# Kernel optimization log

Hardware: AMD Instinct MI355X
Metric: run time of the kernel (lower is better)

Reference implementation:

```python
import jax, jax.numpy as jnp
import numpy as np

QK_I2_S = 128  # weights per block; 32 packed bytes per block
RMS_EPS = 1e-6  # RMSNorm default eps (BitNetMLP builds RMSNorm without eps arg)


def unpack_simd(packed, K):
    """Unpack SIMD block-interleaved 2-bit weights to float {-1,0,1,2}-1 values.

    packed: [M, K//4] uint8. Within each 128-weight block (32 bytes):
      byte[j] bits 6:7 -> w[j+0], 4:5 -> w[j+32], 2:3 -> w[j+64], 0:1 -> w[j+96].
    """
    M = packed.shape[0]
    nb = K // QK_I2_S
    b = packed.astype(jnp.int32).reshape(M, nb, 32)
    # stack shift groups so flattened order is [j+0..31, j+32.., j+64.., j+96..]
    w = jnp.stack([(b >> 6) & 3, (b >> 4) & 3, (b >> 2) & 3, b & 3], axis=2)  # [M,nb,4,32]
    return w.reshape(M, K).astype(jnp.float32) - 1.0


def setup_inputs() -> dict:
    key = jax.random.key(0)
    ks = jax.random.split(key, 8)
    H, I = 2560, 6912
    B, S = 4, 2048
    x = jax.random.normal(ks[0], (B, S, H), dtype=jnp.float32)
    gate_packed = jax.random.randint(ks[1], (I, H // 4), 0, 256, dtype=jnp.int32).astype(jnp.uint8)
    up_packed = jax.random.randint(ks[2], (I, H // 4), 0, 256, dtype=jnp.int32).astype(jnp.uint8)
    down_packed = jax.random.randint(ks[3], (H, I // 4), 0, 256, dtype=jnp.int32).astype(jnp.uint8)
    gate_scale = jax.random.uniform(ks[4], (1,), minval=0.01, maxval=0.1, dtype=jnp.float32)
    up_scale = jax.random.uniform(ks[5], (1,), minval=0.01, maxval=0.1, dtype=jnp.float32)
    down_scale = jax.random.uniform(ks[6], (1,), minval=0.01, maxval=0.1, dtype=jnp.float32)
    norm_w = jnp.ones((I,), dtype=jnp.float32) + 0.05 * jax.random.normal(ks[7], (I,), dtype=jnp.float32)
    return {"x": x, "gate_packed": gate_packed, "gate_scale": gate_scale,
            "up_packed": up_packed, "up_scale": up_scale,
            "down_packed": down_packed, "down_scale": down_scale,
            "norm_w": norm_w}


def reference(x, gate_packed, gate_scale, up_packed, up_scale, down_packed, down_scale, norm_w):
    H = x.shape[-1]
    I = norm_w.shape[0]
    # BitLinear (fallback path math): unpack ternary weights, apply scalar weight scale
    Wg = unpack_simd(gate_packed, H) * gate_scale[0]   # [I, H]
    Wu = unpack_simd(up_packed, H) * up_scale[0]       # [I, H]
    Wd = unpack_simd(down_packed, I) * down_scale[0]   # [H, I]
    gate = jnp.einsum('bsh,ih->bsi', x, Wg)
    up = jnp.einsum('bsh,ih->bsi', x, Wu)
    hidden = jnp.square(jax.nn.relu(gate)) * up        # ReLU^2 gating
    # RMSNorm over intermediate dim
    var = jnp.mean(jnp.square(hidden), axis=-1, keepdims=True)
    hidden = norm_w * (hidden * jax.lax.rsqrt(var + RMS_EPS))
    return jnp.einsum('bsi,hi->bsh', hidden, Wd)
```

## Files before the change

### kernel.cpp

```cpp
#include <hip/hip_runtime.h>
#include <cstdint>
#include <cstddef>

#define H_DIM 2560
#define I_DIM 6912
#define NTOK  8192

typedef __attribute__((ext_vector_type(8))) __bf16 bf16x8;
typedef __attribute__((ext_vector_type(4))) float  f32x4;

__device__ inline void gld16(void* lds, const void* g) {
    __builtin_amdgcn_global_load_lds(
        (__attribute__((address_space(1))) void*)(void*)g,
        (__attribute__((address_space(3))) void*)lds, 16, 0, 0);
}

__global__ __launch_bounds__(256) void cvt_x_kernel(const float* __restrict__ x,
                                                    __bf16* __restrict__ xb, int n8) {
    int gid = blockIdx.x * 256 + threadIdx.x;
    if (gid >= n8) return;
    const float4* p = (const float4*)(x + (size_t)gid * 8);
    float4 v0 = p[0], v1 = p[1];
    bf16x8 o;
    o[0] = (__bf16)v0.x; o[1] = (__bf16)v0.y; o[2] = (__bf16)v0.z; o[3] = (__bf16)v0.w;
    o[4] = (__bf16)v1.x; o[5] = (__bf16)v1.y; o[6] = (__bf16)v1.z; o[7] = (__bf16)v1.w;
    *(bf16x8*)(xb + (size_t)gid * 8) = o;
}

__global__ __launch_bounds__(256) void unpack_w_kernel(const int* __restrict__ packed,
                                                       __bf16* __restrict__ out,
                                                       int M, int K,
                                                       const float* __restrict__ norm,
                                                       int mode) {
    int gid = blockIdx.x * 256 + threadIdx.x;
    int per_row = K >> 3;
    if (gid >= M * per_row) return;
    int i  = gid / per_row;
    int k0 = (gid % per_row) * 8;
    int blk = k0 >> 7;
    int grp = (k0 >> 5) & 3;
    int j0  = k0 & 31;
    int shift = 6 - 2 * grp;
    const int* p = packed + (size_t)i * (K >> 2) + blk * 32 + j0;
    int4 v0 = *(const int4*)p;
    int4 v1 = *(const int4*)(p + 4);
    int vals[8] = {v0.x, v0.y, v0.z, v0.w, v1.x, v1.y, v1.z, v1.w};
    bf16x8 o;
#pragma unroll
    for (int b = 0; b < 8; ++b) {
        float f = (float)(((vals[b] >> shift) & 3) - 1);
        if (norm) f *= norm[k0 + b];
        o[b] = (__bf16)f;
    }
    int dst = (mode == 0) ? i : ((i >> 4) * 32 + (i & 15) + ((mode == 2) ? 16 : 0));
    *(bf16x8*)(out + (size_t)dst * K + k0) = o;
}

__global__ __launch_bounds__(256) void rms_rs_kernel(const __bf16* __restrict__ hidden,
                                                     float* __restrict__ rs) {
    const int tk = blockIdx.x;
    const __bf16* row = hidden + (size_t)tk * I_DIM;
    float s = 0.f;
    for (int idx = threadIdx.x; idx < I_DIM / 8; idx += 256) {
        bf16x8 v = *(const bf16x8*)&row[idx * 8];
#pragma unroll
        for (int j = 0; j < 8; ++j) { float f = (float)v[j]; s += f * f; }
    }
#pragma unroll
    for (int off = 32; off; off >>= 1) s += __shfl_down(s, off, 64);
    __shared__ float wsum[4];
    if ((threadIdx.x & 63) == 0) wsum[threadIdx.x >> 6] = s;
    __syncthreads();
    if (threadIdx.x == 0) {
        float tot = wsum[0] + wsum[1] + wsum[2] + wsum[3];
        rs[tk] = rsqrtf(tot / (float)I_DIM + 1e-6f);
    }
}

template<int KDIM>
__global__ __launch_bounds__(512, 2) void gemm_gu8(
    const __bf16* __restrict__ A,
    const __bf16* __restrict__ B,
    const float* __restrict__ gs_p,
    const float* __restrict__ us_p,
    __bf16* __restrict__ hidden,
    int nby)
{
    constexpr int KB = KDIM * 2;
    constexpr int NT = KDIM / 64;
    __shared__ __align__(16) char smem[131072];

    const int nwg = (int)gridDim.x;
    const int q = nwg >> 3;
    const int id = (int)blockIdx.x;
    const int wg = (id & 7) * q + (id >> 3);
    const int bx = wg / nby, by = wg % nby;
    const int m0 = bx * 256, n0 = by * 256;

    const int t = (int)threadIdx.x;
    const int lane = t & 63;
    const int wid = t >> 6;
    const int wm = wid >> 2, wn = wid & 3;
    const int l15 = lane & 15, s8 = lane >> 4;

    const int qa  = (t & 7) ^ ((t >> 3) & 7);
    const int rA2 = ((t >> 3) << 1) + (qa >> 2);
    const char* gA0 = (const char*)A + (size_t)(m0 + rA2) * KB + (qa & 3) * 16;
    const char* gA1 = (const char*)A + (size_t)(m0 + 128 + rA2) * KB + (qa & 3) * 16;
    const int sr0 = t >> 3, sr1 = 64 + (t >> 3);
    const int br0 = ((sr0 >> 5) << 6) + (sr0 & 31);
    const int br1 = ((sr1 >> 5) << 6) + (sr1 & 31);
    const char* gB0 = (const char*)B + (size_t)(n0 + br0) * KB + qa * 16;
    const char* gB1 = (const char*)B + (size_t)(n0 + br1) * KB + qa * 16;
    char* ldst = smem + t * 16;

    const int aoff = (wm * 64 + (l15 >> 1)) * 128 +
                     (((((l15 & 1) << 2) | s8) ^ ((l15 >> 1) & 7)) << 4);
    const int boff = (wn * 32 + l15) * 128;
    const int bco0 = ((s8) ^ (l15 & 7)) << 4;
    const int bco1 = ((4 | s8) ^ (l15 & 7)) << 4;

    f32x4 acc[8][4];
#pragma unroll
    for (int f = 0; f < 8; ++f)
#pragma unroll
        for (int n = 0; n < 4; ++n) acc[f][n] = (f32x4){0, 0, 0, 0};

#define STG_A(d, kt, kk) do {                                              \
        size_t _oA = (size_t)(kt) * 128 + (kk) * 64;                       \
        gld16(ldst + (d) * 65536 + (kk) * 16384,        gA0 + _oA);        \
        gld16(ldst + (d) * 65536 + (kk) * 16384 + 8192, gA1 + _oA);        \
    } while (0)
#define STG_B(d, kt, nh) do {                                              \
        size_t _oB = (size_t)(nh) * 32 * KB + (size_t)(kt) * 128;          \
        gld16(ldst + (d) * 65536 + 32768 + (nh) * 16384,        gB0 + _oB);\
        gld16(ldst + (d) * 65536 + 32768 + (nh) * 16384 + 8192, gB1 + _oB);\
    } while (0)
#define LOAD_A(d, kk) do { _Pragma("unroll")                               \
        for (int _f = 0; _f < 8; ++_f)                                     \
            a[_f] = *(const bf16x8*)(smem + (d) * 65536 + (kk) * 16384 +   \
                                     _f * 1024 + aoff); } while (0)
#define LOAD_B(d, nh, bc) do {                                             \
        b0 = *(const bf16x8*)(smem + (d) * 65536 + 32768 + (nh) * 16384 +  \
                              boff + (bc));                                \
        b1 = *(const bf16x8*)(smem + (d) * 65536 + 32768 + (nh) * 16384 +  \
                              boff + (bc) + 2048); } while (0)
#define MFMA16(nh) do { __builtin_amdgcn_s_setprio(1); _Pragma("unroll")   \
        for (int _f = 0; _f < 8; ++_f) {                                   \
            acc[_f][(nh) * 2] = __builtin_amdgcn_mfma_f32_16x16x32_bf16(   \
                a[_f], b0, acc[_f][(nh) * 2], 0, 0, 0);                    \
            acc[_f][(nh) * 2 + 1] = __builtin_amdgcn_mfma_f32_16x16x32_bf16(\
                a[_f], b1, acc[_f][(nh) * 2 + 1], 0, 0, 0); }              \
        __builtin_amdgcn_s_setprio(0); } while (0)
#define BAR() do { asm volatile("" ::: "memory");                          \
        __builtin_amdgcn_s_barrier();                                      \
        asm volatile("" ::: "memory"); } while (0)

    STG_A(0, 0, 0); STG_A(0, 0, 1); STG_B(0, 0, 0); STG_B(0, 0, 1);
    STG_A(1, 1, 0); STG_B(1, 1, 0);
    asm volatile("s_waitcnt vmcnt(4)" ::: "memory");
    BAR();

    bf16x8 a[8], b0, b1;
    for (int kt = 0; kt < NT; ++kt) {
        const int d = kt & 1;
        LOAD_A(d, 0); LOAD_B(d, 0, bco0);
        if (kt + 1 < NT) STG_A(d ^ 1, kt + 1, 1);
        BAR(); MFMA16(0); BAR();
        LOAD_B(d, 1, bco0);
        if (kt + 1 < NT) STG_B(d ^ 1, kt + 1, 1);
        BAR(); MFMA16(1); BAR();
        LOAD_A(d, 1); LOAD_B(d, 0, bco1);
        if (kt + 2 < NT) STG_A(d, kt + 2, 0);
        BAR(); MFMA16(0); BAR();
        LOAD_B(d, 1, bco1);
        if (kt + 2 < NT) {
            STG_B(d, kt + 2, 0);
            asm volatile("s_waitcnt vmcnt(4)" ::: "memory");
        } else {
            asm volatile("s_waitcnt vmcnt(0)" ::: "memory");
        }
        BAR(); MFMA16(1); BAR();
    }

#undef STG_A
#undef STG_B
#undef LOAD_A
#undef LOAD_B
#undef MFMA16
#undef BAR

    const float comb = gs_p[0] * gs_p[0] * us_p[0];
    const int r0 = m0 + wm * 128 + s8 * 4;
#pragma unroll
    for (int f = 0; f < 8; ++f)
#pragma unroll
        for (int p = 0; p < 2; ++p)
#pragma unroll
            for (int j = 0; j < 4; ++j) {
                float g = acc[f][2 * p][j];
                float u = acc[f][2 * p + 1][j];
                float r = fmaxf(g, 0.f);
                hidden[(size_t)(r0 + f * 16 + j) * I_DIM +
                       ((by * 8 + wn * 2 + p) * 16 + l15)] = (__bf16)(comb * r * r * u);
            }
}

template<int KDIM>
__global__ __launch_bounds__(512) void gemm_down_pipe(
    const __bf16* __restrict__ A,
    const __bf16* __restrict__ B,
    const float* __restrict__ ds_p,
    const float* __restrict__ rs,
    float* __restrict__ outf,
    int nby)
{
    constexpr int BM = 256, BN = 128, BK = 64;
    constexpr int NT = KDIM / BK;
    constexpr int SLOTB = (BM + BN) * BK * 2;
    __shared__ __align__(16) char smem[3 * SLOTB];

    const int nwg = (int)gridDim.x;
    const int q = nwg >> 3;
    const int id = (int)blockIdx.x;
    const int wg = (id & 7) * q + (id >> 3);
    const int bx = wg / nby;
    const int by = wg % nby;

    const int m0 = bx * BM;
    const int n0 = by * BN;
    const int t  = (int)threadIdx.x;
    const int lane = t & 63;
    const int wm = (t >> 6) >> 1;
    const int wn = (t >> 6) & 1;

    const int srow = t >> 3;
    const int scol = ((t & 7) * 16) ^ ((srow & 7) << 4);
    const char* gA = (const char*)A + (size_t)(m0 + srow) * (KDIM * 2) + scol;
    const char* gB = (const char*)B + (size_t)(n0 + srow) * (KDIM * 2) + scol;
    char* lbase = smem + t * 16;

    const int l15 = lane & 15;
    const int xv  = (l15 & 7) << 4;
    const int colx[2] = { (((lane >> 4) * 16) ^ xv), ((64 + (lane >> 4) * 16) ^ xv) };

    f32x4 acc[4][4];
#pragma unroll
    for (int a = 0; a < 4; ++a)
#pragma unroll
        for (int b = 0; b < 4; ++b) acc[a][b] = (f32x4){0, 0, 0, 0};

#define STAGE_T(s, kt) do {                                                     \
        char* _ls = lbase + (s) * SLOTB;                                        \
        const char* _ga = gA + (kt) * (BK * 2);                                 \
        _Pragma("unroll")                                                       \
        for (int _i = 0; _i < 4; ++_i)                                          \
            gld16(_ls + _i * 8192, _ga + (size_t)_i * 64 * (KDIM * 2));         \
        const char* _gb = gB + (kt) * (BK * 2);                                 \
        char* _lb = _ls + BM * BK * 2;                                          \
        _Pragma("unroll")                                                       \
        for (int _i = 0; _i < 2; ++_i)                                          \
            gld16(_lb + _i * 8192, _gb + (size_t)_i * 64 * (KDIM * 2));         \
    } while (0)

#define COMPUTE_T(s) do {                                                       \
        const char* _sa = smem + (s) * SLOTB;                                   \
        const char* _sb = _sa + BM * BK * 2;                                    \
        _Pragma("unroll")                                                       \
        for (int _kk = 0; _kk < 2; ++_kk) {                                     \
            bf16x8 _a[4], _b[4];                                                \
            _Pragma("unroll")                                                   \
            for (int _f = 0; _f < 4; ++_f)                                      \
                _a[_f] = *(const bf16x8*)(_sa + (wm * 64 + _f * 16 + l15) * 128 + colx[_kk]); \
            _Pragma("unroll")                                                   \
            for (int _f = 0; _f < 4; ++_f)                                      \
                _b[_f] = *(const bf16x8*)(_sb + (wn * 64 + _f * 16 + l15) * 128 + colx[_kk]); \
            __builtin_amdgcn_s_setprio(1);                                      \
            _Pragma("unroll")                                                   \
            for (int _fm = 0; _fm < 4; ++_fm)                                   \
                _Pragma("unroll")                                               \
                for (int _fn = 0; _fn < 4; ++_fn)                               \
                    acc[_fm][_fn] = __builtin_amdgcn_mfma_f32_16x16x32_bf16(    \
                        _a[_fm], _b[_fn], acc[_fm][_fn], 0, 0, 0);              \
            __builtin_amdgcn_s_setprio(0);                                      \
        }                                                                       \
    } while (0)

    STAGE_T(0, 0);
    STAGE_T(1, 1);
    asm volatile("s_waitcnt vmcnt(6)" ::: "memory");
    __builtin_amdgcn_s_barrier();
    asm volatile("" ::: "memory");

    for (int kt = 0; kt < NT; ++kt) {
        if (kt + 2 < NT) STAGE_T((kt + 2) % 3, kt + 2);
        COMPUTE_T(kt % 3);
        if (kt + 2 < NT) {
            asm volatile("s_waitcnt vmcnt(6)" ::: "memory");
            __builtin_amdgcn_s_barrier();
            asm volatile("" ::: "memory");
        } else if (kt + 2 == NT) {
            asm volatile("s_waitcnt vmcnt(0)" ::: "memory");
            __builtin_amdgcn_s_barrier();
            asm volatile("" ::: "memory");
        }
    }

#undef STAGE_T
#undef COMPUTE_T

    const float ds = ds_p[0];
    const int r0 = m0 + wm * 64 + (lane >> 4) * 4;
#pragma unroll
    for (int fm = 0; fm < 4; ++fm)
#pragma unroll
        for (int j = 0; j < 4; ++j) {
            const int row = r0 + fm * 16 + j;
            const float sc = ds * rs[row];
#pragma unroll
            for (int fn = 0; fn < 4; ++fn)
                outf[(size_t)row * H_DIM + (n0 + wn * 64 + fn * 16 + l15)] =
                    sc * acc[fm][fn][j];
        }
}

extern "C" void kernel_launch(void* const* d_in, const int* in_sizes, int n_in,
                              void* d_out, int out_size, void* d_ws, size_t ws_size,
                              hipStream_t stream) {
    const float* x   = (const float*)d_in[0];
    const int*   gp  = (const int*)d_in[1];
    const float* gs  = (const float*)d_in[2];
    const int*   upk = (const int*)d_in[3];
    const float* us  = (const float*)d_in[4];
    const int*   dp  = (const int*)d_in[5];
    const float* dsc = (const float*)d_in[6];
    const float* nw  = (const float*)d_in[7];
    float* out = (float*)d_out;

    char* ws = (char*)d_ws;
    __bf16* xb     = (__bf16*)ws;  ws += (size_t)NTOK * H_DIM * 2;
    __bf16* bgu    = (__bf16*)ws;  ws += (size_t)2 * I_DIM * H_DIM * 2;
    __bf16* wdb    = (__bf16*)ws;  ws += (size_t)H_DIM * I_DIM * 2;
    __bf16* hidden = (__bf16*)ws;  ws += (size_t)NTOK * I_DIM * 2;
    float*  rsbuf  = (float*)ws;   ws += (size_t)NTOK * 4;

    cvt_x_kernel<<<(NTOK * H_DIM / 8 + 255) / 256, 256, 0, stream>>>(x, xb, NTOK * H_DIM / 8);
    unpack_w_kernel<<<(I_DIM * H_DIM / 8 + 255) / 256, 256, 0, stream>>>(gp, bgu, I_DIM, H_DIM, nullptr, 1);
    unpack_w_kernel<<<(I_DIM * H_DIM / 8 + 255) / 256, 256, 0, stream>>>(upk, bgu, I_DIM, H_DIM, nullptr, 2);
    unpack_w_kernel<<<(H_DIM * I_DIM / 8 + 255) / 256, 256, 0, stream>>>(dp, wdb, H_DIM, I_DIM, nw, 0);

    gemm_gu8<H_DIM><<<dim3((NTOK / 256) * (2 * I_DIM / 256)), 512, 0, stream>>>(
        xb, bgu, gs, us, hidden, 2 * I_DIM / 256);

    rms_rs_kernel<<<NTOK, 256, 0, stream>>>(hidden, rsbuf);

    gemm_down_pipe<I_DIM><<<dim3((NTOK / 256) * (H_DIM / 128)), 512, 0, stream>>>(
        hidden, wdb, dsc, rsbuf, out, H_DIM / 128);
}
```

Before: 855.4 us.

## Switch both GEMMs to 32x32x16 MFMA with matching interleave and LDS layout

Both the gate/up GEMM and the down GEMM now use the 32x32x16 bf16 MFMA instead of 16x16x32. The gate/up weights are interleaved in 32-row groups to match the larger tile. LDS fragment addressing, the staging order and the epilogue row mapping are rewritten for the 32x32 output layout. The larger MFMA does more work per instruction and needs fewer LDS reads per flop. In exchange it changes register pressure and the LDS bank access pattern, and the swizzle must stay correct.

```diff
diff --git a/kernel.cpp b/kernel.cpp
--- a/kernel.cpp
+++ b/kernel.cpp
@@ -8,6 +8,7 @@
 
 typedef __attribute__((ext_vector_type(8))) __bf16 bf16x8;
 typedef __attribute__((ext_vector_type(4))) float  f32x4;
+typedef __attribute__((ext_vector_type(16))) float f32x16;
 
 __device__ inline void gld16(void* lds, const void* g) {
     __builtin_amdgcn_global_load_lds(
@@ -52,7 +53,7 @@
         if (norm) f *= norm[k0 + b];
         o[b] = (__bf16)f;
     }
-    int dst = (mode == 0) ? i : ((i >> 4) * 32 + (i & 15) + ((mode == 2) ? 16 : 0));
+    int dst = (mode == 0) ? i : ((i >> 5) * 64 + (i & 31) + ((mode == 2) ? 32 : 0));
     *(bf16x8*)(out + (size_t)dst * K + k0) = o;
 }
 
@@ -78,7 +79,7 @@
 }
 
 template<int KDIM>
-__global__ __launch_bounds__(512, 2) void gemm_gu8(
+__global__ __launch_bounds__(512, 2) void gemm_gu32(
     const __bf16* __restrict__ A,
     const __bf16* __restrict__ B,
     const float* __restrict__ gs_p,
@@ -101,59 +102,69 @@
     const int lane = t & 63;
     const int wid = t >> 6;
     const int wm = wid >> 2, wn = wid & 3;
-    const int l15 = lane & 15, s8 = lane >> 4;
+    const int l31 = lane & 31, lh = lane >> 5;
 
     const int qa  = (t & 7) ^ ((t >> 3) & 7);
     const int rA2 = ((t >> 3) << 1) + (qa >> 2);
-    const char* gA0 = (const char*)A + (size_t)(m0 + rA2) * KB + (qa & 3) * 16;
-    const char* gA1 = (const char*)A + (size_t)(m0 + 128 + rA2) * KB + (qa & 3) * 16;
-    const int sr0 = t >> 3, sr1 = 64 + (t >> 3);
-    const int br0 = ((sr0 >> 5) << 6) + (sr0 & 31);
-    const int br1 = ((sr1 >> 5) << 6) + (sr1 & 31);
-    const char* gB0 = (const char*)B + (size_t)(n0 + br0) * KB + qa * 16;
-    const char* gB1 = (const char*)B + (size_t)(n0 + br1) * KB + qa * 16;
+    const int cb  = (qa & 3) * 16;
+    const char* gA0 = (const char*)A + (size_t)(m0 + rA2) * KB + cb;
+    const char* gA1 = (const char*)A + (size_t)(m0 + 128 + rA2) * KB + cb;
+    const char* gB0 = (const char*)B + (size_t)(n0 + rA2) * KB + cb;
+    const char* gB1 = (const char*)B + (size_t)(n0 + 128 + rA2) * KB + cb;
     char* ldst = smem + t * 16;
 
-    const int aoff = (wm * 64 + (l15 >> 1)) * 128 +
-                     (((((l15 & 1) << 2) | s8) ^ ((l15 >> 1) & 7)) << 4);
-    const int boff = (wn * 32 + l15) * 128;
-    const int bco0 = ((s8) ^ (l15 & 7)) << 4;
-    const int bco1 = ((4 | s8) ^ (l15 & 7)) << 4;
-
-    f32x4 acc[8][4];
-#pragma unroll
-    for (int f = 0; f < 8; ++f)
-#pragma unroll
-        for (int n = 0; n < 4; ++n) acc[f][n] = (f32x4){0, 0, 0, 0};
-
-#define STG_A(d, kt, kk) do {                                              \
-        size_t _oA = (size_t)(kt) * 128 + (kk) * 64;                       \
-        gld16(ldst + (d) * 65536 + (kk) * 16384,        gA0 + _oA);        \
-        gld16(ldst + (d) * 65536 + (kk) * 16384 + 8192, gA1 + _oA);        \
-    } while (0)
-#define STG_B(d, kt, nh) do {                                              \
-        size_t _oB = (size_t)(nh) * 32 * KB + (size_t)(kt) * 128;          \
-        gld16(ldst + (d) * 65536 + 32768 + (nh) * 16384,        gB0 + _oB);\
-        gld16(ldst + (d) * 65536 + 32768 + (nh) * 16384 + 8192, gB1 + _oB);\
-    } while (0)
-#define LOAD_A(d, kk) do { _Pragma("unroll")                               \
-        for (int _f = 0; _f < 8; ++_f)                                     \
-            a[_f] = *(const bf16x8*)(smem + (d) * 65536 + (kk) * 16384 +   \
-                                     _f * 1024 + aoff); } while (0)
-#define LOAD_B(d, nh, bc) do {                                             \
-        b0 = *(const bf16x8*)(smem + (d) * 65536 + 32768 + (nh) * 16384 +  \
-                              boff + (bc));                                \
-        b1 = *(const bf16x8*)(smem + (d) * 65536 + 32768 + (nh) * 16384 +  \
-                              boff + (bc) + 2048); } while (0)
-#define MFMA16(nh) do { __builtin_amdgcn_s_setprio(1); _Pragma("unroll")   \
-        for (int _f = 0; _f < 8; ++_f) {                                   \
-            acc[_f][(nh) * 2] = __builtin_amdgcn_mfma_f32_16x16x32_bf16(   \
-                a[_f], b0, acc[_f][(nh) * 2], 0, 0, 0);                    \
-            acc[_f][(nh) * 2 + 1] = __builtin_amdgcn_mfma_f32_16x16x32_bf16(\
-                a[_f], b1, acc[_f][(nh) * 2 + 1], 0, 0, 0); }              \
+    const int abase = (wm * 64 + (l31 >> 1)) * 128;
+    const int bbase = (wn * 32 + (l31 >> 1)) * 128;
+    const int xr = (lane >> 1) & 7;
+    const int sl0 = ((((lane & 1) << 2) | (0 + lh)) ^ xr) << 4;
+    const int sl1 = ((((lane & 1) << 2) | (2 + lh)) ^ xr) << 4;
+
+    f32x16 acc[4][2];
+#pragma unroll
+    for (int mf = 0; mf < 4; ++mf)
+#pragma unroll
+        for (int nf = 0; nf < 2; ++nf)
+#pragma unroll
+            for (int r = 0; r < 16; ++r) acc[mf][nf][r] = 0.f;
+
+#define STG_A(d, kt, kk) do {                                                  \
+        gld16(ldst + (d) * 65536 + (kk) * 16384,                               \
+              gA0 + (size_t)(kt) * 128 + (kk) * 64);                           \
+        gld16(ldst + (d) * 65536 + (kk) * 16384 + 8192,                        \
+              gA1 + (size_t)(kt) * 128 + (kk) * 64);                           \
+    } while (0)
+#define STG_B(d, kt, kk) do {                                                  \
+        gld16(ldst + (d) * 65536 + 32768 + (kk) * 16384,                       \
+              gB0 + (size_t)(kt) * 128 + (kk) * 64);                           \
+        gld16(ldst + (d) * 65536 + 32768 + (kk) * 16384 + 8192,                \
+              gB1 + (size_t)(kt) * 128 + (kk) * 64);                           \
+    } while (0)
+#define PHASE_LOAD(d, kk) do {                                                 \
+        const char* _ba = smem + (d) * 65536 + (kk) * 16384;                   \
+        _Pragma("unroll")                                                      \
+        for (int _mf = 0; _mf < 4; ++_mf) {                                    \
+            a[_mf][0] = *(const bf16x8*)(_ba + abase + _mf * 2048 + sl0);      \
+            a[_mf][1] = *(const bf16x8*)(_ba + abase + _mf * 2048 + sl1);      \
+        }                                                                      \
+        const char* _bb = smem + (d) * 65536 + 32768 + (kk) * 16384;           \
+        _Pragma("unroll")                                                      \
+        for (int _nf = 0; _nf < 2; ++_nf) {                                    \
+            b[_nf][0] = *(const bf16x8*)(_bb + bbase + _nf * 2048 + sl0);      \
+            b[_nf][1] = *(const bf16x8*)(_bb + bbase + _nf * 2048 + sl1);      \
+        }                                                                      \
+    } while (0)
+#define PHASE_MMA() do { __builtin_amdgcn_s_setprio(1);                        \
+        _Pragma("unroll")                                                      \
+        for (int _ks = 0; _ks < 2; ++_ks)                                      \
+        _Pragma("unroll")                                                      \
+        for (int _mf = 0; _mf < 4; ++_mf)                                      \
+        _Pragma("unroll")                                                      \
+        for (int _nf = 0; _nf < 2; ++_nf)                                      \
+            acc[_mf][_nf] = __builtin_amdgcn_mfma_f32_32x32x16_bf16(           \
+                a[_mf][_ks], b[_nf][_ks], acc[_mf][_nf], 0, 0, 0);             \
         __builtin_amdgcn_s_setprio(0); } while (0)
-#define BAR() do { asm volatile("" ::: "memory");                          \
-        __builtin_amdgcn_s_barrier();                                      \
+#define BAR() do { asm volatile("" ::: "memory");                              \
+        __builtin_amdgcn_s_barrier();                                          \
         asm volatile("" ::: "memory"); } while (0)
 
     STG_A(0, 0, 0); STG_A(0, 0, 1); STG_B(0, 0, 0); STG_B(0, 0, 1);
@@ -161,49 +172,41 @@
     asm volatile("s_waitcnt vmcnt(4)" ::: "memory");
     BAR();
 
-    bf16x8 a[8], b0, b1;
+    bf16x8 a[4][2], b[2][2];
     for (int kt = 0; kt < NT; ++kt) {
         const int d = kt & 1;
-        LOAD_A(d, 0); LOAD_B(d, 0, bco0);
-        if (kt + 1 < NT) STG_A(d ^ 1, kt + 1, 1);
-        BAR(); MFMA16(0); BAR();
-        LOAD_B(d, 1, bco0);
-        if (kt + 1 < NT) STG_B(d ^ 1, kt + 1, 1);
-        BAR(); MFMA16(1); BAR();
-        LOAD_A(d, 1); LOAD_B(d, 0, bco1);
-        if (kt + 2 < NT) STG_A(d, kt + 2, 0);
-        BAR(); MFMA16(0); BAR();
-        LOAD_B(d, 1, bco1);
+        PHASE_LOAD(d, 0);
+        if (kt + 1 < NT) { STG_B(d ^ 1, kt + 1, 1); STG_A(d ^ 1, kt + 1, 1); }
+        BAR(); PHASE_MMA(); BAR();
+        PHASE_LOAD(d, 1);
         if (kt + 2 < NT) {
-            STG_B(d, kt + 2, 0);
+            STG_A(d, kt + 2, 0); STG_B(d, kt + 2, 0);
             asm volatile("s_waitcnt vmcnt(4)" ::: "memory");
         } else {
             asm volatile("s_waitcnt vmcnt(0)" ::: "memory");
         }
-        BAR(); MFMA16(1); BAR();
+        BAR(); PHASE_MMA(); BAR();
     }
 
 #undef STG_A
 #undef STG_B
-#undef LOAD_A
-#undef LOAD_B
-#undef MFMA16
+#undef PHASE_LOAD
+#undef PHASE_MMA
 #undef BAR
 
     const float comb = gs_p[0] * gs_p[0] * us_p[0];
-    const int r0 = m0 + wm * 128 + s8 * 4;
-#pragma unroll
-    for (int f = 0; f < 8; ++f)
-#pragma unroll
-        for (int p = 0; p < 2; ++p)
-#pragma unroll
-            for (int j = 0; j < 4; ++j) {
-                float g = acc[f][2 * p][j];
-                float u = acc[f][2 * p + 1][j];
-                float r = fmaxf(g, 0.f);
-                hidden[(size_t)(r0 + f * 16 + j) * I_DIM +
-                       ((by * 8 + wn * 2 + p) * 16 + l15)] = (__bf16)(comb * r * r * u);
-            }
+    const int colg = by * 128 + wn * 32 + l31;
+#pragma unroll
+    for (int mf = 0; mf < 4; ++mf)
+#pragma unroll
+        for (int reg = 0; reg < 16; ++reg) {
+            const int rowl = (reg & 3) + 8 * (reg >> 2) + 4 * lh;
+            const int row = m0 + wm * 128 + mf * 32 + rowl;
+            float g = acc[mf][0][reg];
+            float u = acc[mf][1][reg];
+            float r = fmaxf(g, 0.f);
+            hidden[(size_t)row * I_DIM + colg] = (__bf16)(comb * r * r * u);
+        }
 }
 
 template<int KDIM>
@@ -233,6 +236,8 @@
     const int lane = t & 63;
     const int wm = (t >> 6) >> 1;
     const int wn = (t >> 6) & 1;
+    const int l31 = lane & 31, lh = lane >> 5;
+    const int sx = lane & 7;
 
     const int srow = t >> 3;
     const int scol = ((t & 7) * 16) ^ ((srow & 7) << 4);
@@ -240,15 +245,13 @@
     const char* gB = (const char*)B + (size_t)(n0 + srow) * (KDIM * 2) + scol;
     char* lbase = smem + t * 16;
 
-    const int l15 = lane & 15;
-    const int xv  = (l15 & 7) << 4;
-    const int colx[2] = { (((lane >> 4) * 16) ^ xv), ((64 + (lane >> 4) * 16) ^ xv) };
-
-    f32x4 acc[4][4];
-#pragma unroll
-    for (int a = 0; a < 4; ++a)
-#pragma unroll
-        for (int b = 0; b < 4; ++b) acc[a][b] = (f32x4){0, 0, 0, 0};
+    f32x16 acc[2][2];
+#pragma unroll
+    for (int mf = 0; mf < 2; ++mf)
+#pragma unroll
+        for (int nf = 0; nf < 2; ++nf)
+#pragma unroll
+            for (int r = 0; r < 16; ++r) acc[mf][nf][r] = 0.f;
 
 #define STAGE_T(s, kt) do {                                                     \
         char* _ls = lbase + (s) * SLOTB;                                        \
@@ -267,21 +270,17 @@
         const char* _sa = smem + (s) * SLOTB;                                   \
         const char* _sb = _sa + BM * BK * 2;                                    \
         _Pragma("unroll")                                                       \
-        for (int _kk = 0; _kk < 2; ++_kk) {                                     \
-            bf16x8 _a[4], _b[4];                                                \
-            _Pragma("unroll")                                                   \
-            for (int _f = 0; _f < 4; ++_f)                                      \
-                _a[_f] = *(const bf16x8*)(_sa + (wm * 64 + _f * 16 + l15) * 128 + colx[_kk]); \
-            _Pragma("unroll")                                                   \
-            for (int _f = 0; _f < 4; ++_f)                                      \
-                _b[_f] = *(const bf16x8*)(_sb + (wn * 64 + _f * 16 + l15) * 128 + colx[_kk]); \
+        for (int _ks = 0; _ks < 4; ++_ks) {                                     \
+            const int _so = (((_ks * 2 + lh) ^ sx) << 4);                       \
+            bf16x8 _a0 = *(const bf16x8*)(_sa + (wm * 64 + l31) * 128 + _so);   \
+            bf16x8 _a1 = *(const bf16x8*)(_sa + (wm * 64 + 32 + l31) * 128 + _so); \
+            bf16x8 _b0 = *(const bf16x8*)(_sb + (wn * 64 + l31) * 128 + _so);   \
+            bf16x8 _b1 = *(const bf16x8*)(_sb + (wn * 64 + 32 + l31) * 128 + _so); \
             __builtin_amdgcn_s_setprio(1);                                      \
-            _Pragma("unroll")                                                   \
-            for (int _fm = 0; _fm < 4; ++_fm)                                   \
-                _Pragma("unroll")                                               \
-                for (int _fn = 0; _fn < 4; ++_fn)                               \
-                    acc[_fm][_fn] = __builtin_amdgcn_mfma_f32_16x16x32_bf16(    \
-                        _a[_fm], _b[_fn], acc[_fm][_fn], 0, 0, 0);              \
+            acc[0][0] = __builtin_amdgcn_mfma_f32_32x32x16_bf16(_a0, _b0, acc[0][0], 0, 0, 0); \
+            acc[0][1] = __builtin_amdgcn_mfma_f32_32x32x16_bf16(_a0, _b1, acc[0][1], 0, 0, 0); \
+            acc[1][0] = __builtin_amdgcn_mfma_f32_32x32x16_bf16(_a1, _b0, acc[1][0], 0, 0, 0); \
+            acc[1][1] = __builtin_amdgcn_mfma_f32_32x32x16_bf16(_a1, _b1, acc[1][1], 0, 0, 0); \
             __builtin_amdgcn_s_setprio(0);                                      \
         }                                                                       \
     } while (0)
@@ -310,17 +309,17 @@
 #undef COMPUTE_T
 
     const float ds = ds_p[0];
-    const int r0 = m0 + wm * 64 + (lane >> 4) * 4;
-#pragma unroll
-    for (int fm = 0; fm < 4; ++fm)
-#pragma unroll
-        for (int j = 0; j < 4; ++j) {
-            const int row = r0 + fm * 16 + j;
+#pragma unroll
+    for (int mf = 0; mf < 2; ++mf)
+#pragma unroll
+        for (int reg = 0; reg < 16; ++reg) {
+            const int rowl = (reg & 3) + 8 * (reg >> 2) + 4 * lh;
+            const int row = m0 + wm * 64 + mf * 32 + rowl;
             const float sc = ds * rs[row];
 #pragma unroll
-            for (int fn = 0; fn < 4; ++fn)
-                outf[(size_t)row * H_DIM + (n0 + wn * 64 + fn * 16 + l15)] =
-                    sc * acc[fm][fn][j];
+            for (int nf = 0; nf < 2; ++nf)
+                outf[(size_t)row * H_DIM + (n0 + wn * 64 + nf * 32 + l31)] =
+                    sc * acc[mf][nf][reg];
         }
 }
 
@@ -349,7 +348,7 @@
     unpack_w_kernel<<<(I_DIM * H_DIM / 8 + 255) / 256, 256, 0, stream>>>(upk, bgu, I_DIM, H_DIM, nullptr, 2);
     unpack_w_kernel<<<(H_DIM * I_DIM / 8 + 255) / 256, 256, 0, stream>>>(dp, wdb, H_DIM, I_DIM, nw, 0);
 
-    gemm_gu8<H_DIM><<<dim3((NTOK / 256) * (2 * I_DIM / 256)), 512, 0, stream>>>(
+    gemm_gu32<H_DIM><<<dim3((NTOK / 256) * (2 * I_DIM / 256)), 512, 0, stream>>>(
         xb, bgu, gs, us, hidden, 2 * I_DIM / 256);
 
     rms_rs_kernel<<<NTOK, 256, 0, stream>>>(hidden, rsbuf);
```

New measurement: 956.6 us. +11.8%, slower.
